# Kernel optimization log

Hardware: AMD Instinct MI355X
Metric: run time of the kernel (lower is better)

Reference implementation:

```python
import jax, jax.numpy as jnp
import numpy as np

NUM_NODE = 5000
EMBED_DIM = 256
NUM_CLS = 20
EDGE_ROWS = (NUM_NODE - 1) * (NUM_NODE - 1) + 1  # 24990002
BZ, SEQ, NBR = 64, 512, 16


def setup_inputs() -> dict:
    key = jax.random.key(0)
    k = jax.random.split(key, 8)
    X = jax.random.randint(k[0], (BZ, SEQ), 0, NUM_NODE)
    NX = jax.random.randint(k[1], (BZ, SEQ, NBR), 0, NUM_NODE)
    EW = jax.random.randint(k[2], (BZ, SEQ, NBR), 0, EDGE_ROWS)
    # parameters (xavier-ish scale); padding_idx=0 rows zeroed
    node_emb = jax.random.normal(k[3], (NUM_NODE, EMBED_DIM), jnp.float32) * 0.02
    node_emb = node_emb.at[0].set(0.0)
    edge_w = jax.random.normal(k[4], (EDGE_ROWS, 1), jnp.float32) * 0.02
    edge_w = edge_w.at[0].set(0.0)
    node_w = jax.random.normal(k[5], (NUM_NODE, 1), jnp.float32) * 0.02
    node_w = node_w.at[0].set(0.0)
    fc_W = jax.random.normal(k[6], (NUM_CLS, EMBED_DIM), jnp.float32) * 0.05
    fc_b = jnp.zeros((NUM_CLS,), jnp.float32)
    return {"X": X, "NX": NX, "EW": EW, "node_emb": node_emb,
            "edge_w": edge_w, "node_w": node_w, "fc_W": fc_W, "fc_b": fc_b}


def reference(X, NX, EW, node_emb, edge_w, node_w, fc_W, fc_b):
    Ra = node_emb[NX]                      # (bz, seq, nbr, d) neighbor embeddings
    Ean = edge_w[EW]                       # (bz, seq, nbr, 1) edge weights
    Mn = jnp.max(Ra * Ean, axis=2)         # (bz, seq, d) max over neighbors
    Rn = node_emb[X]                       # (bz, seq, d)
    Nn = node_w[X]                         # (bz, seq, 1)
    y = (1.0 - Nn) * Mn + Nn * Rn          # weighted combine
    y = jnp.sum(y, axis=1)                 # (bz, d) sum-pool over sequence
    y = y @ fc_W.T + fc_b                  # (bz, num_cls)
    y = jax.nn.relu(y)
    # Dropout is identity at inference; LogSoftmax over dim=1
    return jax.nn.log_softmax(y, axis=1)
```

## Files before the change

### kernel.cpp

```cpp
#include <hip/hip_runtime.h>
#include <math.h>

#define NUM_NODE 5000
#define BZ   64
#define SEQ  512
#define NBR  16
#define DIM  256
#define NCLS 20

#define SEQ_PER_BLOCK 16
#define NCHUNK (SEQ / SEQ_PER_BLOCK)
#define ROWB  (DIM * 2)

__device__ __forceinline__ int bcast_i(int v, int lane) {
    return __builtin_amdgcn_readlane(v, lane);
}
__device__ __forceinline__ float bcast_f(float v, int lane) {
    return __int_as_float(__builtin_amdgcn_readlane(__float_as_int(v), lane));
}
__device__ __forceinline__ unsigned bf16_rne(float f) {
    unsigned u = __float_as_uint(f);
    return (u + 0x7fffu + ((u >> 16) & 1u)) >> 16;
}
__device__ __forceinline__ float lo_bf16(unsigned u) { return __uint_as_float(u << 16); }
__device__ __forceinline__ float hi_bf16(unsigned u) { return __uint_as_float(u & 0xffff0000u); }

__global__ __launch_bounds__(256) void zero_ws_kernel(float* __restrict__ ws, int n) {
    int i = blockIdx.x * blockDim.x + threadIdx.x;
    if (i < n) ws[i] = 0.0f;
}

__global__ __launch_bounds__(256) void cvt_emb_kernel(
    const float4* __restrict__ src, uint2* __restrict__ dst, int n4) {
    int i = blockIdx.x * blockDim.x + threadIdx.x;
    if (i < n4) {
        float4 v = src[i];
        uint2 o;
        o.x = bf16_rne(v.x) | (bf16_rne(v.y) << 16);
        o.y = bf16_rne(v.z) | (bf16_rne(v.w) << 16);
        dst[i] = o;
    }
}

__global__ __launch_bounds__(256, 4) void gnn_gather_kernel(
    const int*   __restrict__ X,
    const int*   __restrict__ NX,
    const int*   __restrict__ EW,
    const float* __restrict__ node_emb,
    const char*  __restrict__ embb,
    const float* __restrict__ edge_w,
    const float* __restrict__ node_w,
    float*       __restrict__ dst)
{
    __shared__ float lds[4][DIM];

    const int b     = blockIdx.x / NCHUNK;
    const int chunk = blockIdx.x % NCHUNK;
    const int wave  = threadIdx.x >> 6;
    const int lane  = threadIdx.x & 63;
    const int half  = lane >> 5;
    const int sub   = lane & 31;
    const int voff  = sub * 16;

    const int s0  = chunk * SEQ_PER_BLOCK + wave * 4;
    const int bs0 = b * SEQ + s0;

    const int   nx  = __builtin_nontemporal_load(&NX[bs0 * NBR + lane]);
    const int   ewi = __builtin_nontemporal_load(&EW[bs0 * NBR + lane]);
    const float ew  = __builtin_nontemporal_load(&edge_w[ewi]);

    int   xv  = 0;
    float nwv = 0.f;
    if (lane < 4) {
        xv  = X[bs0 + lane];
        nwv = node_w[xv];
    }

    float acc[8] = {0.f, 0.f, 0.f, 0.f, 0.f, 0.f, 0.f, 0.f};

    #pragma unroll
    for (int p = 0; p < 4; ++p) {
        float m[8];
        #pragma unroll
        for (int i = 0; i < 8; ++i) m[i] = -INFINITY;

        #pragma unroll
        for (int j = 0; j < 8; ++j) {
            const int   n0 = bcast_i(nx, p * 16 + 2 * j);
            const int   n1 = bcast_i(nx, p * 16 + 2 * j + 1);
            const float w0 = bcast_f(ew, p * 16 + 2 * j);
            const float w1 = bcast_f(ew, p * 16 + 2 * j + 1);
            const int   n  = half ? n1 : n0;
            const float w  = half ? w1 : w0;
            const uint4 e  = *(const uint4*)(embb + ((size_t)n * ROWB) + voff);
            m[0] = fmaxf(m[0], lo_bf16(e.x) * w);
            m[1] = fmaxf(m[1], hi_bf16(e.x) * w);
            m[2] = fmaxf(m[2], lo_bf16(e.y) * w);
            m[3] = fmaxf(m[3], hi_bf16(e.y) * w);
            m[4] = fmaxf(m[4], lo_bf16(e.z) * w);
            m[5] = fmaxf(m[5], hi_bf16(e.z) * w);
            m[6] = fmaxf(m[6], lo_bf16(e.w) * w);
            m[7] = fmaxf(m[7], hi_bf16(e.w) * w);
        }

        #pragma unroll
        for (int i = 0; i < 8; ++i)
            m[i] = fmaxf(m[i], __shfl_xor(m[i], 32));

        const int   x  = bcast_i(xv, p);
        const float nn = bcast_f(nwv, p);
        const float om = 1.0f - nn;
        const float4 ra = *(const float4*)(node_emb + (size_t)x * DIM + 8 * sub);
        const float4 rb = *(const float4*)(node_emb + (size_t)x * DIM + 8 * sub + 4);
        acc[0] += om * m[0] + nn * ra.x;
        acc[1] += om * m[1] + nn * ra.y;
        acc[2] += om * m[2] + nn * ra.z;
        acc[3] += om * m[3] + nn * ra.w;
        acc[4] += om * m[4] + nn * rb.x;
        acc[5] += om * m[5] + nn * rb.y;
        acc[6] += om * m[6] + nn * rb.z;
        acc[7] += om * m[7] + nn * rb.w;
    }

    if (half == 0) {
        *(float4*)&lds[wave][8 * sub]     = make_float4(acc[0], acc[1], acc[2], acc[3]);
        *(float4*)&lds[wave][8 * sub + 4] = make_float4(acc[4], acc[5], acc[6], acc[7]);
    }
    __syncthreads();

    const int t = threadIdx.x;
    dst[((size_t)b * NCHUNK + chunk) * DIM + t] =
        lds[0][t] + lds[1][t] + lds[2][t] + lds[3][t];
}

__global__ __launch_bounds__(256) void gnn_gather_f32_kernel(
    const int*   __restrict__ X,
    const int*   __restrict__ NX,
    const int*   __restrict__ EW,
    const float* __restrict__ node_emb,
    const float* __restrict__ edge_w,
    const float* __restrict__ node_w,
    float*       __restrict__ dst)
{
    __shared__ float lds[4][DIM];
    const int b     = blockIdx.x / NCHUNK;
    const int chunk = blockIdx.x % NCHUNK;
    const int wave  = threadIdx.x >> 6;
    const int lane  = threadIdx.x & 63;
    const int s0  = chunk * SEQ_PER_BLOCK + wave * 4;
    const int bs0 = b * SEQ + s0;

    const int   nx  = NX[bs0 * NBR + lane];
    const float ew  = edge_w[EW[bs0 * NBR + lane]];
    int xv = 0; float nwv = 0.f;
    if (lane < 4) { xv = X[bs0 + lane]; nwv = node_w[xv]; }

    float4 acc = make_float4(0.f, 0.f, 0.f, 0.f);
    for (int p = 0; p < 4; ++p) {
        float4 m = make_float4(-INFINITY, -INFINITY, -INFINITY, -INFINITY);
        for (int k = 0; k < NBR; ++k) {
            const int   n = bcast_i(nx, p * 16 + k);
            const float w = bcast_f(ew, p * 16 + k);
            const float4 e = *(const float4*)(node_emb + (size_t)n * DIM + 4 * lane);
            m.x = fmaxf(m.x, e.x * w); m.y = fmaxf(m.y, e.y * w);
            m.z = fmaxf(m.z, e.z * w); m.w = fmaxf(m.w, e.w * w);
        }
        const int   x  = bcast_i(xv, p);
        const float nn = bcast_f(nwv, p);
        const float om = 1.0f - nn;
        const float4 r = *(const float4*)(node_emb + (size_t)x * DIM + 4 * lane);
        acc.x += om * m.x + nn * r.x; acc.y += om * m.y + nn * r.y;
        acc.z += om * m.z + nn * r.z; acc.w += om * m.w + nn * r.w;
    }
    *(float4*)&lds[wave][4 * lane] = acc;
    __syncthreads();
    const int t = threadIdx.x;
    atomicAdd(&dst[b * DIM + t], lds[0][t] + lds[1][t] + lds[2][t] + lds[3][t]);
}

__global__ __launch_bounds__(256) void gnn_head_kernel(
    const float* __restrict__ part,
    const float* __restrict__ fc_W,
    const float* __restrict__ fc_b,
    float*       __restrict__ out,
    int nslots)
{
    __shared__ float yrow[DIM];
    __shared__ float vals[NCLS];
    __shared__ float lse;

    const int b = blockIdx.x;
    const int t = threadIdx.x;

    float sum = 0.f;
    for (int c = 0; c < nslots; ++c)
        sum += part[((size_t)b * nslots + c) * DIM + t];
    yrow[t] = sum;
    __syncthreads();

    const int wave = t >> 6;
    const int lane = t & 63;
    const float4 y4 = *(const float4*)&yrow[4 * lane];

    #pragma unroll
    for (int ci = 0; ci < 5; ++ci) {
        const int c = wave * 5 + ci;
        const float4 w4 = *(const float4*)(fc_W + c * DIM + 4 * lane);
        float d = y4.x * w4.x + y4.y * w4.y + y4.z * w4.z + y4.w * w4.w;
        #pragma unroll
        for (int off = 32; off; off >>= 1) d += __shfl_xor(d, off);
        if (lane == 0) vals[c] = fmaxf(d + fc_b[c], 0.0f);
    }
    __syncthreads();

    if (t == 0) {
        float mx = -INFINITY;
        for (int c = 0; c < NCLS; ++c) mx = fmaxf(mx, vals[c]);
        float s = 0.0f;
        for (int c = 0; c < NCLS; ++c) s += expf(vals[c] - mx);
        lse = mx + logf(s);
    }
    __syncthreads();

    if (t < NCLS) out[b * NCLS + t] = vals[t] - lse;
}

extern "C" void kernel_launch(void* const* d_in, const int* in_sizes, int n_in,
                              void* d_out, int out_size, void* d_ws, size_t ws_size,
                              hipStream_t stream) {
    const int*   X        = (const int*)  d_in[0];
    const int*   NX       = (const int*)  d_in[1];
    const int*   EW       = (const int*)  d_in[2];
    const float* node_emb = (const float*)d_in[3];
    const float* edge_w   = (const float*)d_in[4];
    const float* node_w   = (const float*)d_in[5];
    const float* fc_W     = (const float*)d_in[6];
    const float* fc_b     = (const float*)d_in[7];
    float* out = (float*)d_out;

    const size_t part_bytes = (size_t)BZ * NCHUNK * DIM * sizeof(float);
    const size_t emb_bytes  = (size_t)NUM_NODE * DIM * sizeof(unsigned short);
    float* part = (float*)d_ws;
    char*  embb = (char*)d_ws + part_bytes;

    if (ws_size >= part_bytes + emb_bytes) {
        const int n4 = NUM_NODE * DIM / 4;
        cvt_emb_kernel<<<(n4 + 255) / 256, 256, 0, stream>>>(
            (const float4*)node_emb, (uint2*)embb, n4);
        gnn_gather_kernel<<<BZ * NCHUNK, 256, 0, stream>>>(
            X, NX, EW, node_emb, embb, edge_w, node_w, part);
        gnn_head_kernel<<<BZ, 256, 0, stream>>>(part, fc_W, fc_b, out, NCHUNK);
    } else {
        zero_ws_kernel<<<(BZ * DIM + 255) / 256, 256, 0, stream>>>(part, BZ * DIM);
        gnn_gather_f32_kernel<<<BZ * NCHUNK, 256, 0, stream>>>(
            X, NX, EW, node_emb, edge_w, node_w, part);
        gnn_head_kernel<<<BZ, 256, 0, stream>>>(part, fc_W, fc_b, out, 1);
    }
}
```

Measured before the change: 183.2 us.

## Assign one sequence position per wave and batch all neighbor loads upfront

```diff
diff --git a/kernel.cpp b/kernel.cpp
--- a/kernel.cpp
+++ b/kernel.cpp
@@ -8,9 +8,9 @@
 #define DIM  256
 #define NCLS 20
 
-#define SEQ_PER_BLOCK 16
-#define NCHUNK (SEQ / SEQ_PER_BLOCK)
 #define ROWB  (DIM * 2)
+#define NCHUNK2 (SEQ / 4)
+#define NCHUNK16 (SEQ / 16)
 
 __device__ __forceinline__ int bcast_i(int v, int lane) {
     return __builtin_amdgcn_readlane(v, lane);
@@ -46,7 +46,6 @@
     const int*   __restrict__ X,
     const int*   __restrict__ NX,
     const int*   __restrict__ EW,
-    const float* __restrict__ node_emb,
     const char*  __restrict__ embb,
     const float* __restrict__ edge_w,
     const float* __restrict__ node_w,
@@ -54,73 +53,70 @@
 {
     __shared__ float lds[4][DIM];
 
-    const int b     = blockIdx.x / NCHUNK;
-    const int chunk = blockIdx.x % NCHUNK;
+    const int b     = blockIdx.x / NCHUNK2;
+    const int chunk = blockIdx.x % NCHUNK2;
     const int wave  = threadIdx.x >> 6;
     const int lane  = threadIdx.x & 63;
     const int half  = lane >> 5;
     const int sub   = lane & 31;
     const int voff  = sub * 16;
 
-    const int s0  = chunk * SEQ_PER_BLOCK + wave * 4;
-    const int bs0 = b * SEQ + s0;
-
-    const int   nx  = __builtin_nontemporal_load(&NX[bs0 * NBR + lane]);
-    const int   ewi = __builtin_nontemporal_load(&EW[bs0 * NBR + lane]);
-    const float ew  = __builtin_nontemporal_load(&edge_w[ewi]);
-
-    int   xv  = 0;
-    float nwv = 0.f;
-    if (lane < 4) {
-        xv  = X[bs0 + lane];
-        nwv = node_w[xv];
-    }
-
-    float acc[8] = {0.f, 0.f, 0.f, 0.f, 0.f, 0.f, 0.f, 0.f};
-
-    #pragma unroll
-    for (int p = 0; p < 4; ++p) {
-        float m[8];
-        #pragma unroll
-        for (int i = 0; i < 8; ++i) m[i] = -INFINITY;
-
-        #pragma unroll
-        for (int j = 0; j < 8; ++j) {
-            const int   n0 = bcast_i(nx, p * 16 + 2 * j);
-            const int   n1 = bcast_i(nx, p * 16 + 2 * j + 1);
-            const float w0 = bcast_f(ew, p * 16 + 2 * j);
-            const float w1 = bcast_f(ew, p * 16 + 2 * j + 1);
-            const int   n  = half ? n1 : n0;
-            const float w  = half ? w1 : w0;
-            const uint4 e  = *(const uint4*)(embb + ((size_t)n * ROWB) + voff);
-            m[0] = fmaxf(m[0], lo_bf16(e.x) * w);
-            m[1] = fmaxf(m[1], hi_bf16(e.x) * w);
-            m[2] = fmaxf(m[2], lo_bf16(e.y) * w);
-            m[3] = fmaxf(m[3], hi_bf16(e.y) * w);
-            m[4] = fmaxf(m[4], lo_bf16(e.z) * w);
-            m[5] = fmaxf(m[5], hi_bf16(e.z) * w);
-            m[6] = fmaxf(m[6], lo_bf16(e.w) * w);
-            m[7] = fmaxf(m[7], hi_bf16(e.w) * w);
-        }
-
-        #pragma unroll
-        for (int i = 0; i < 8; ++i)
-            m[i] = fmaxf(m[i], __shfl_xor(m[i], 32));
-
-        const int   x  = bcast_i(xv, p);
-        const float nn = bcast_f(nwv, p);
-        const float om = 1.0f - nn;
-        const float4 ra = *(const float4*)(node_emb + (size_t)x * DIM + 8 * sub);
-        const float4 rb = *(const float4*)(node_emb + (size_t)x * DIM + 8 * sub + 4);
-        acc[0] += om * m[0] + nn * ra.x;
-        acc[1] += om * m[1] + nn * ra.y;
-        acc[2] += om * m[2] + nn * ra.z;
-        acc[3] += om * m[3] + nn * ra.w;
-        acc[4] += om * m[4] + nn * rb.x;
-        acc[5] += om * m[5] + nn * rb.y;
-        acc[6] += om * m[6] + nn * rb.z;
-        acc[7] += om * m[7] + nn * rb.w;
-    }
+    const int s  = chunk * 4 + wave;
+    const int bs = b * SEQ + s;
+
+    int   nxv = 0;
+    float ewv = 0.f;
+    if (lane < NBR) {
+        nxv = __builtin_nontemporal_load(&NX[bs * NBR + lane]);
+        const int ewi = __builtin_nontemporal_load(&EW[bs * NBR + lane]);
+        ewv = __builtin_nontemporal_load(&edge_w[ewi]);
+    }
+    const int   x  = X[bs];
+    const float nn = node_w[x];
+
+    uint4 e[8];
+    #pragma unroll
+    for (int j = 0; j < 8; ++j) {
+        const int n0 = bcast_i(nxv, 2 * j);
+        const int n1 = bcast_i(nxv, 2 * j + 1);
+        const int n  = half ? n1 : n0;
+        e[j] = *(const uint4*)(embb + (size_t)n * ROWB + voff);
+    }
+    const uint4 es = *(const uint4*)(embb + (size_t)x * ROWB + voff);
+
+    float m[8];
+    #pragma unroll
+    for (int i = 0; i < 8; ++i) m[i] = -INFINITY;
+
+    #pragma unroll
+    for (int j = 0; j < 8; ++j) {
+        const float w0 = bcast_f(ewv, 2 * j);
+        const float w1 = bcast_f(ewv, 2 * j + 1);
+        const float w  = half ? w1 : w0;
+        m[0] = fmaxf(m[0], lo_bf16(e[j].x) * w);
+        m[1] = fmaxf(m[1], hi_bf16(e[j].x) * w);
+        m[2] = fmaxf(m[2], lo_bf16(e[j].y) * w);
+        m[3] = fmaxf(m[3], hi_bf16(e[j].y) * w);
+        m[4] = fmaxf(m[4], lo_bf16(e[j].z) * w);
+        m[5] = fmaxf(m[5], hi_bf16(e[j].z) * w);
+        m[6] = fmaxf(m[6], lo_bf16(e[j].w) * w);
+        m[7] = fmaxf(m[7], hi_bf16(e[j].w) * w);
+    }
+
+    #pragma unroll
+    for (int i = 0; i < 8; ++i)
+        m[i] = fmaxf(m[i], __shfl_xor(m[i], 32));
+
+    const float om = 1.0f - nn;
+    float acc[8];
+    acc[0] = om * m[0] + nn * lo_bf16(es.x);
+    acc[1] = om * m[1] + nn * hi_bf16(es.x);
+    acc[2] = om * m[2] + nn * lo_bf16(es.y);
+    acc[3] = om * m[3] + nn * hi_bf16(es.y);
+    acc[4] = om * m[4] + nn * lo_bf16(es.z);
+    acc[5] = om * m[5] + nn * hi_bf16(es.z);
+    acc[6] = om * m[6] + nn * lo_bf16(es.w);
+    acc[7] = om * m[7] + nn * hi_bf16(es.w);
 
     if (half == 0) {
         *(float4*)&lds[wave][8 * sub]     = make_float4(acc[0], acc[1], acc[2], acc[3]);
@@ -129,7 +125,7 @@
     __syncthreads();
 
     const int t = threadIdx.x;
-    dst[((size_t)b * NCHUNK + chunk) * DIM + t] =
+    dst[(size_t)blockIdx.x * DIM + t] =
         lds[0][t] + lds[1][t] + lds[2][t] + lds[3][t];
 }
 
@@ -143,11 +139,11 @@
     float*       __restrict__ dst)
 {
     __shared__ float lds[4][DIM];
-    const int b     = blockIdx.x / NCHUNK;
-    const int chunk = blockIdx.x % NCHUNK;
+    const int b     = blockIdx.x / NCHUNK16;
+    const int chunk = blockIdx.x % NCHUNK16;
     const int wave  = threadIdx.x >> 6;
     const int lane  = threadIdx.x & 63;
-    const int s0  = chunk * SEQ_PER_BLOCK + wave * 4;
+    const int s0  = chunk * 16 + wave * 4;
     const int bs0 = b * SEQ + s0;
 
     const int   nx  = NX[bs0 * NBR + lane];
@@ -193,6 +189,7 @@
     const int t = threadIdx.x;
 
     float sum = 0.f;
+    #pragma unroll 4
     for (int c = 0; c < nslots; ++c)
         sum += part[((size_t)b * nslots + c) * DIM + t];
     yrow[t] = sum;
@@ -238,7 +235,7 @@
     const float* fc_b     = (const float*)d_in[7];
     float* out = (float*)d_out;
 
-    const size_t part_bytes = (size_t)BZ * NCHUNK * DIM * sizeof(float);
+    const size_t part_bytes = (size_t)BZ * NCHUNK2 * DIM * sizeof(float);
     const size_t emb_bytes  = (size_t)NUM_NODE * DIM * sizeof(unsigned short);
     float* part = (float*)d_ws;
     char*  embb = (char*)d_ws + part_bytes;
@@ -247,12 +244,12 @@
         const int n4 = NUM_NODE * DIM / 4;
         cvt_emb_kernel<<<(n4 + 255) / 256, 256, 0, stream>>>(
             (const float4*)node_emb, (uint2*)embb, n4);
-        gnn_gather_kernel<<<BZ * NCHUNK, 256, 0, stream>>>(
-            X, NX, EW, node_emb, embb, edge_w, node_w, part);
-        gnn_head_kernel<<<BZ, 256, 0, stream>>>(part, fc_W, fc_b, out, NCHUNK);
+        gnn_gather_kernel<<<BZ * NCHUNK2, 256, 0, stream>>>(
+            X, NX, EW, embb, edge_w, node_w, part);
+        gnn_head_kernel<<<BZ, 256, 0, stream>>>(part, fc_W, fc_b, out, NCHUNK2);
     } else {
         zero_ws_kernel<<<(BZ * DIM + 255) / 256, 256, 0, stream>>>(part, BZ * DIM);
-        gnn_gather_f32_kernel<<<BZ * NCHUNK, 256, 0, stream>>>(
+        gnn_gather_f32_kernel<<<BZ * NCHUNK16, 256, 0, stream>>>(
             X, NX, EW, node_emb, edge_w, node_w, part);
         gnn_head_kernel<<<BZ, 256, 0, stream>>>(part, fc_W, fc_b, out, 1);
     }
```

Result: no change. 182.1 us (-0.6%).
